# Kernel tuning notes

Measured on AMD Instinct MI355X. Metric: run time of the kernel, lower is better.

## Reference

```python
import jax, jax.numpy as jnp
import numpy as np

# Module hyperparameters (init_kwargs): shape_data = [n_t, n_y, n_x]
N_T, N_Y, N_X = 5, 32, 32
N = N_Y * N_X            # nb_nodes
DX = DY = DT = 1.0


def setup_inputs() -> dict:
    key = jax.random.key(0)
    k1, k2, k3 = jax.random.split(key, 3)
    n_b = 4
    kappa = jax.random.uniform(k1, (n_b, 1, N, N_T), dtype=jnp.float32)
    m = jax.random.normal(k2, (n_b, 2, N, N_T), dtype=jnp.float32)
    H = jax.random.normal(k3, (n_b, 2, 2, N, N_T), dtype=jnp.float32)
    return {"kappa": kappa, "m": m, "H": H}


def _stencil_indices():
    # 9-point stencil on the n_y x n_x grid; row-major node index = y*n_x + x.
    yy, xx = np.meshgrid(np.arange(N_Y), np.arange(N_X), indexing="ij")
    yy, xx = yy.reshape(-1), xx.reshape(-1)
    node = np.arange(N)
    offs = [(0, 0), (0, 1), (0, -1), (1, 0), (-1, 0), (1, 1), (1, -1), (-1, 1), (-1, -1)]
    rows, cols, valid = [], [], []
    for oy, ox in offs:
        ny, nx = yy + oy, xx + ox
        ok = (ny >= 0) & (ny < N_Y) & (nx >= 0) & (nx < N_X)
        rows.append(node)
        cols.append(np.where(ok, ny * N_X + nx, node))
        valid.append(ok.astype(np.float32))
    return (jnp.asarray(np.concatenate(rows)),
            jnp.asarray(np.concatenate(cols)),
            jnp.asarray(np.concatenate(valid)))

ROWS, COLS, VALID = _stencil_indices()


def _build_A(kappa, m, H):
    # Finite-difference discretization of A = kappa^2 I + m.grad - div(H grad)
    # kappa: [b,t,N]; m: [b,t,2,N]; H: [b,t,2,2,N]
    mx, my = m[..., 0, :], m[..., 1, :]
    H11, H22 = H[..., 0, 0, :], H[..., 1, 1, :]
    H12 = 0.5 * (H[..., 0, 1, :] + H[..., 1, 0, :])
    c0 = kappa ** 2 + 2.0 * H11 / DX ** 2 + 2.0 * H22 / DY ** 2   # center
    cpx = mx / (2 * DX) - H11 / DX ** 2                           # (0,+1)
    cmx = -mx / (2 * DX) - H11 / DX ** 2                          # (0,-1)
    cpy = my / (2 * DY) - H22 / DY ** 2                           # (+1,0)
    cmy = -my / (2 * DY) - H22 / DY ** 2                          # (-1,0)
    cc = H12 / (2 * DX * DY)                                      # cross term
    # order matches _stencil_indices offsets
    vals = jnp.concatenate([c0, cpx, cmx, cpy, cmy, -cc, cc, cc, -cc], axis=-1)
    vals = vals * VALID                                           # zero out-of-grid neighbors
    b, t = vals.shape[0], vals.shape[1]
    A = jnp.zeros((b, t, N, N), vals.dtype)
    return A.at[:, :, ROWS, COLS].add(vals)


def reference(kappa, m, H):
    # rearrange to [batch, time, ...] leading
    kap = jnp.transpose(kappa[:, 0], (0, 2, 1))          # [b,t,N]
    mm = jnp.transpose(m, (0, 3, 1, 2))                  # [b,t,2,N]
    HH = jnp.transpose(H, (0, 4, 1, 2, 3))               # [b,t,2,2,N]
    A = _build_A(kap, mm, HH)                            # [b,t,N,N]
    I = jnp.eye(N, dtype=A.dtype)
    M = I + DT * A                                       # M_k = Id + dt * A_k
    MM = jnp.einsum("btij,btjk->btik", M, M)             # spspmm(M_k, M_k)
    b = M.shape[0]
    Q = jnp.zeros((b, N_T * N, N_T * N), A.dtype)
    # block-tridiagonal precision matrix assembly (QR = Id)
    Q = Q.at[:, 0:N, 0:N].set(MM[:, 0])
    Q = Q.at[:, 0:N, N:2 * N].set(-M[:, 1])
    for i in range(1, N_T - 1):
        Q = Q.at[:, i * N:(i + 1) * N, (i - 1) * N:i * N].set(-M[:, i - 1])
        Q = Q.at[:, i * N:(i + 1) * N, i * N:(i + 1) * N].set(MM[:, i] + I)
        Q = Q.at[:, i * N:(i + 1) * N, (i + 1) * N:(i + 2) * N].set(-M[:, i + 1])
    i = N_T - 1
    Q = Q.at[:, i * N:(i + 1) * N, (i - 1) * N:i * N].set(-M[:, i - 1])
    Q = Q.at[:, i * N:(i + 1) * N, i * N:(i + 1) * N].set(MM[:, i])
    return Q
```

## Files before the change

### kernel.cpp

```cpp
#include <hip/hip_runtime.h>

#define NT   5
#define NY   32
#define NX   32
#define NN   1024
#define QDIM 5120
#define NB   4

__device__ const int c_oy[9] = {0, 0, 0, 1, -1, 1, 1, -1, -1};
__device__ const int c_ox[9] = {0, 1, -1, 0, 0, 1, -1, 1, -1};

__device__ __forceinline__ void stencil9(const float* __restrict__ kap,
                                         const float* __restrict__ m,
                                         const float* __restrict__ H,
                                         int b, int t, int n, float s[9]) {
    float k   = kap[((size_t)b * NN + n) * NT + t];
    float mx  = m[(((size_t)b * 2 + 0) * NN + n) * NT + t];
    float my  = m[(((size_t)b * 2 + 1) * NN + n) * NT + t];
    float H11 = H[((((size_t)b * 2 + 0) * 2 + 0) * NN + n) * NT + t];
    float H01 = H[((((size_t)b * 2 + 0) * 2 + 1) * NN + n) * NT + t];
    float H10 = H[((((size_t)b * 2 + 1) * 2 + 0) * NN + n) * NT + t];
    float H22 = H[((((size_t)b * 2 + 1) * 2 + 1) * NN + n) * NT + t];
    float cc = 0.25f * (H01 + H10);
    s[0] = 1.0f + k * k + 2.0f * H11 + 2.0f * H22;
    s[1] =  0.5f * mx - H11;
    s[2] = -0.5f * mx - H11;
    s[3] =  0.5f * my - H22;
    s[4] = -0.5f * my - H22;
    s[5] = -cc;
    s[6] =  cc;
    s[7] =  cc;
    s[8] = -cc;
    int y = n >> 5, x = n & 31;
    if (x == NX - 1) { s[1] = 0.f; s[5] = 0.f; s[7] = 0.f; }
    if (x == 0)      { s[2] = 0.f; s[6] = 0.f; s[8] = 0.f; }
    if (y == NY - 1) { s[3] = 0.f; s[5] = 0.f; s[6] = 0.f; }
    if (y == 0)      { s[4] = 0.f; s[7] = 0.f; s[8] = 0.f; }
}

__global__ __launch_bounds__(256) void spde_fused(const float* __restrict__ kap,
                                                  const float* __restrict__ m,
                                                  const float* __restrict__ H,
                                                  float* __restrict__ Q) {
    const int oy[9] = {0, 0, 0, 1, -1, 1, 1, -1, -1};
    const int ox[9] = {0, 1, -1, 0, 0, 1, -1, 1, -1};

    int row = blockIdx.x;
    int b = row / (NT * NN);
    int g = row - b * (NT * NN);
    int t = g >> 10;
    int r = g & (NN - 1);
    int ry = r >> 5, rx = r & 31;
    int tid = threadIdx.x;

    __shared__ float sk[9][9];
    __shared__ float moff[2][9];
    __shared__ float accL[25];

    if (tid < 9) {
        int ky = ry + c_oy[tid], kx = rx + c_ox[tid];
        bool valid = ((unsigned)ky < NY) && ((unsigned)kx < NX);
        int k = valid ? (ky * NX + kx) : r;
        float s[9];
        stencil9(kap, m, H, b, t, k, s);
#pragma unroll
        for (int e = 0; e < 9; ++e)
            sk[tid][(oy[e] + 1) * 3 + (ox[e] + 1)] = s[e];
    } else if (tid == 9) {
        float s[9] = {0,0,0,0,0,0,0,0,0};
        if (t >= 1) stencil9(kap, m, H, b, t - 1, r, s);
#pragma unroll
        for (int e = 0; e < 9; ++e)
            moff[0][(oy[e] + 1) * 3 + (ox[e] + 1)] = -s[e];
    } else if (tid == 10) {
        float s[9] = {0,0,0,0,0,0,0,0,0};
        if (t <= NT - 2) stencil9(kap, m, H, b, t + 1, r, s);
#pragma unroll
        for (int e = 0; e < 9; ++e)
            moff[1][(oy[e] + 1) * 3 + (ox[e] + 1)] = -s[e];
    }
    __syncthreads();

    if (tid < 25) {
        int dy = tid / 5 - 2, dx = tid % 5 - 2;
        float a = 0.f;
#pragma unroll
        for (int d1 = 0; d1 < 9; ++d1) {
            int dy2 = dy - oy[d1], dx2 = dx - ox[d1];
            if (dy2 >= -1 && dy2 <= 1 && dx2 >= -1 && dx2 <= 1) {
                a += sk[0][(oy[d1] + 1) * 3 + (ox[d1] + 1)]
                   * sk[d1][(dy2 + 1) * 3 + (dx2 + 1)];
            }
        }
        if (tid == 12 && t >= 1 && t <= NT - 2) a += 1.0f;
        accL[tid] = a;
    }
    __syncthreads();

    size_t base = ((size_t)b * QDIM + g) * QDIM;
#pragma unroll
    for (int kk = 0; kk < 5; ++kk) {
        int slot = tid + kk * 256;
        int c0 = slot * 4;
        int j  = c0 >> 10;
        int o  = c0 & (NN - 1);
        int dy = (o >> 5) - ry;
        int dx0 = (o & 31) - rx;
        float4 v = make_float4(0.f, 0.f, 0.f, 0.f);
        float* ve = &v.x;
        if (j == t) {
            if (dy >= -2 && dy <= 2) {
#pragma unroll
                for (int e = 0; e < 4; ++e) {
                    int dx = dx0 + e;
                    if (dx >= -2 && dx <= 2) ve[e] = accL[(dy + 2) * 5 + (dx + 2)];
                }
            }
        } else if ((j == t - 1 || j == t + 1) && dy >= -1 && dy <= 1) {
            int z = (j > t) ? 1 : 0;
#pragma unroll
            for (int e = 0; e < 4; ++e) {
                int dx = dx0 + e;
                if (dx >= -1 && dx <= 1) ve[e] = moff[z][(dy + 1) * 3 + (dx + 1)];
            }
        }
        *(float4*)(Q + base + c0) = v;
    }
}

extern "C" void kernel_launch(void* const* d_in, const int* in_sizes, int n_in,
                              void* d_out, int out_size, void* d_ws, size_t ws_size,
                              hipStream_t stream) {
    const float* kap = (const float*)d_in[0];
    const float* m   = (const float*)d_in[1];
    const float* H   = (const float*)d_in[2];
    float* Q = (float*)d_out;

    int nrows = NB * NT * NN;
    spde_fused<<<nrows, 256, 0, stream>>>(kap, m, H, Q);
}
```

Before: 417.6 us.

## Zero output with memset and scatter only nonzero stencil entries

Instead of having each block write a full dense row of Q, including all the zeros, the output is cleared up front with hipMemsetAsync. The kernel then only scatters the up to 43 nonzero entries per row, using 64-thread blocks. The aim is to let the memset engine or fill kernel handle the bulk zero traffic at full bandwidth, and to cut the main kernel down to tiny scattered stores. It adds a second operation on the stream and uses uncoalesced scalar stores, and total DRAM write traffic for Q stays about the same.

```diff
diff --git a/kernel.cpp b/kernel.cpp
--- a/kernel.cpp
+++ b/kernel.cpp
@@ -38,10 +38,10 @@
     if (y == 0)      { s[4] = 0.f; s[7] = 0.f; s[8] = 0.f; }
 }
 
-__global__ __launch_bounds__(256) void spde_fused(const float* __restrict__ kap,
-                                                  const float* __restrict__ m,
-                                                  const float* __restrict__ H,
-                                                  float* __restrict__ Q) {
+__global__ __launch_bounds__(64) void spde_scatter(const float* __restrict__ kap,
+                                                   const float* __restrict__ m,
+                                                   const float* __restrict__ H,
+                                                   float* __restrict__ Q) {
     const int oy[9] = {0, 0, 0, 1, -1, 1, 1, -1, -1};
     const int ox[9] = {0, 1, -1, 0, 0, 1, -1, 1, -1};
 
@@ -70,14 +70,12 @@
         float s[9] = {0,0,0,0,0,0,0,0,0};
         if (t >= 1) stencil9(kap, m, H, b, t - 1, r, s);
 #pragma unroll
-        for (int e = 0; e < 9; ++e)
-            moff[0][(oy[e] + 1) * 3 + (ox[e] + 1)] = -s[e];
+        for (int e = 0; e < 9; ++e) moff[0][e] = -s[e];
     } else if (tid == 10) {
         float s[9] = {0,0,0,0,0,0,0,0,0};
         if (t <= NT - 2) stencil9(kap, m, H, b, t + 1, r, s);
 #pragma unroll
-        for (int e = 0; e < 9; ++e)
-            moff[1][(oy[e] + 1) * 3 + (ox[e] + 1)] = -s[e];
+        for (int e = 0; e < 9; ++e) moff[1][e] = -s[e];
     }
     __syncthreads();
 
@@ -97,34 +95,27 @@
     }
     __syncthreads();
 
-    size_t base = ((size_t)b * QDIM + g) * QDIM;
-#pragma unroll
-    for (int kk = 0; kk < 5; ++kk) {
-        int slot = tid + kk * 256;
-        int c0 = slot * 4;
-        int j  = c0 >> 10;
-        int o  = c0 & (NN - 1);
-        int dy = (o >> 5) - ry;
-        int dx0 = (o & 31) - rx;
-        float4 v = make_float4(0.f, 0.f, 0.f, 0.f);
-        float* ve = &v.x;
-        if (j == t) {
-            if (dy >= -2 && dy <= 2) {
-#pragma unroll
-                for (int e = 0; e < 4; ++e) {
-                    int dx = dx0 + e;
-                    if (dx >= -2 && dx <= 2) ve[e] = accL[(dy + 2) * 5 + (dx + 2)];
-                }
-            }
-        } else if ((j == t - 1 || j == t + 1) && dy >= -1 && dy <= 1) {
-            int z = (j > t) ? 1 : 0;
-#pragma unroll
-            for (int e = 0; e < 4; ++e) {
-                int dx = dx0 + e;
-                if (dx >= -1 && dx <= 1) ve[e] = moff[z][(dy + 1) * 3 + (dx + 1)];
-            }
+    size_t rowbase = ((size_t)b * QDIM + g) * QDIM;
+
+    if (tid < 25) {
+        int dy = tid / 5 - 2, dx = tid % 5 - 2;
+        int cy = ry + dy, cx = rx + dx;
+        if ((unsigned)cy < NY && (unsigned)cx < NX)
+            Q[rowbase + (size_t)t * NN + cy * NX + cx] = accL[tid];
+    } else if (tid >= 32 && tid < 41) {
+        if (t >= 1) {
+            int d = tid - 32;
+            int cy = ry + c_oy[d], cx = rx + c_ox[d];
+            if ((unsigned)cy < NY && (unsigned)cx < NX)
+                Q[rowbase + (size_t)(t - 1) * NN + cy * NX + cx] = moff[0][d];
         }
-        *(float4*)(Q + base + c0) = v;
+    } else if (tid >= 48 && tid < 57) {
+        if (t <= NT - 2) {
+            int d = tid - 48;
+            int cy = ry + c_oy[d], cx = rx + c_ox[d];
+            if ((unsigned)cy < NY && (unsigned)cx < NX)
+                Q[rowbase + (size_t)(t + 1) * NN + cy * NX + cx] = moff[1][d];
+        }
     }
 }
 
@@ -136,6 +127,8 @@
     const float* H   = (const float*)d_in[2];
     float* Q = (float*)d_out;
 
+    hipMemsetAsync(d_out, 0, (size_t)out_size * sizeof(float), stream);
+
     int nrows = NB * NT * NN;
-    spde_fused<<<nrows, 256, 0, stream>>>(kap, m, H, Q);
+    spde_scatter<<<nrows, 64, 0, stream>>>(kap, m, H, Q);
 }
```

Measured after the change: 436.1 us. 4.4% more time.
